# Optimization experiments

Measured on AMD Instinct MI355X. Metric: run time of the kernel, lower is better.

The kernel has to match this reference:

```python
import jax, jax.numpy as jnp
import numpy as np

N = 1_500_000
CB, CT, CO, B = 96, 128, 96, 8
BN_EPS = 1e-5


def setup_inputs() -> dict:
    key = jax.random.key(0)
    k1, k2, k3, k4 = jax.random.split(key, 4)
    return {
        "backbone_F": jax.random.normal(k1, (N, CB), dtype=jnp.float32),
        "batch_idx": jax.random.randint(k2, (N,), 0, B, dtype=jnp.int32),
        "text_feats": jax.random.normal(k3, (B, CT), dtype=jnp.float32),
        "W": jax.random.normal(k4, (CB + CT, CO), dtype=jnp.float32) * (1.0 / np.sqrt(CB + CT)),
        "gamma": jnp.ones((CO,), dtype=jnp.float32),
        "beta": jnp.zeros((CO,), dtype=jnp.float32),
    }


def reference(backbone_F, batch_idx, text_feats, W, gamma, beta):
    # gather text feats per point via batch index: [N, CT]
    rep_text = text_feats[batch_idx]
    # concat backbone + text feats: [N, CB+CT]
    combined = jnp.concatenate([backbone_F, rep_text], axis=1)
    # 1x1 sparse conv == pointwise GEMM (no bias): [N, CO]
    x = combined @ W
    # BatchNorm (training mode: batch stats over the N points)
    mean = jnp.mean(x, axis=0)
    var = jnp.var(x, axis=0)
    x = (x - mean) * jax.lax.rsqrt(var + BN_EPS) * gamma + beta
    # ReLU
    return jnp.maximum(x, 0.0)
```

## Files before the change

### kernel.cpp

```cpp
#include <hip/hip_runtime.h>
#include <hip/hip_bf16.h>

#define N_PTS 1500000
#define CBCH 96
#define CTCH 128
#define COCH 96
#define NB 8
#define BN_EPS 1e-5f

#define GSUM_OFF 0
#define GSQ_OFF 96
#define T_OFF 384

typedef __attribute__((ext_vector_type(8))) short bf16x8;
typedef __attribute__((ext_vector_type(4))) float f32x4;

__device__ __forceinline__ unsigned short f2bf_rne(float f) {
    union { float f; unsigned u; } v; v.f = f;
    unsigned u = v.u;
    return (unsigned short)((u + 0x7FFFu + ((u >> 16) & 1u)) >> 16);
}

__global__ void k0_init(const float* __restrict__ text, const float* __restrict__ W,
                        float* __restrict__ ws) {
    if (blockIdx.x == NB) {
        for (int i = threadIdx.x; i < 192; i += blockDim.x) ws[i] = 0.f;
        return;
    }
    int b = blockIdx.x;
    int c = threadIdx.x;
    if (c < COCH) {
        float acc = 0.f;
        #pragma unroll 8
        for (int k = 0; k < CTCH; ++k)
            acc += text[b * CTCH + k] * W[(CBCH + k) * COCH + c];
        ws[T_OFF + b * COCH + c] = acc;
    }
}


__device__ __forceinline__ void load_bfrag(const float* __restrict__ W, int grp, int lr,
                                           bf16x8 bf[6][3]) {
    #pragma unroll
    for (int ct = 0; ct < 6; ++ct)
        #pragma unroll
        for (int kt = 0; kt < 3; ++kt)
            #pragma unroll
            for (int j = 0; j < 8; ++j)
                bf[ct][kt][j] = (short)f2bf_rne(W[(kt * 32 + grp * 8 + j) * COCH + ct * 16 + lr]);
}

__global__ __launch_bounds__(256, 2) void k1_stats(const float* __restrict__ bb,
                                                   const int* __restrict__ bidx,
                                                   const float* __restrict__ W,
                                                   float* __restrict__ ws) {
    __shared__ float sT[NB * COCH];
    __shared__ float sred[2][4][COCH];
    for (int i = threadIdx.x; i < NB * COCH; i += blockDim.x) sT[i] = ws[T_OFF + i];
    __syncthreads();

    const int lane = threadIdx.x & 63;
    const int wv = threadIdx.x >> 6;
    const int grp = lane >> 4, lr = lane & 15;

    bf16x8 bf[6][3];
    load_bfrag(W, grp, lr, bf);

    float sum[6] = {0.f, 0.f, 0.f, 0.f, 0.f, 0.f};
    float sq[6] = {0.f, 0.f, 0.f, 0.f, 0.f, 0.f};

    const int gw = blockIdx.x * 4 + wv;
    const int nw = gridDim.x * 4;
    const int NT = N_PTS / 16;
    for (int t = gw; t < NT; t += nw) {
        int base = t * 16;
        f32x4 acc[6];
        #pragma unroll
        for (int r = 0; r < 4; ++r) {
            int b = bidx[base + grp * 4 + r];
            #pragma unroll
            for (int ct = 0; ct < 6; ++ct)
                acc[ct][r] = sT[b * COCH + ct * 16 + lr];
        }
        bf16x8 af[3];
        #pragma unroll
        for (int kt = 0; kt < 3; ++kt) {
            const f32x4* p = reinterpret_cast<const f32x4*>(bb + (size_t)(base + lr) * CBCH + kt * 32 + grp * 8);
            f32x4 x0 = p[0], x1 = p[1];
            #pragma unroll
            for (int j = 0; j < 4; ++j) {
                af[kt][j]     = (short)f2bf_rne(x0[j]);
                af[kt][4 + j] = (short)f2bf_rne(x1[j]);
            }
        }
        #pragma unroll
        for (int ct = 0; ct < 6; ++ct)
            #pragma unroll
            for (int kt = 0; kt < 3; ++kt)
                acc[ct] = __builtin_amdgcn_mfma_f32_16x16x32_bf16(af[kt], bf[ct][kt], acc[ct], 0, 0, 0);
        #pragma unroll
        for (int ct = 0; ct < 6; ++ct)
            #pragma unroll
            for (int r = 0; r < 4; ++r) {
                float x = acc[ct][r];
                sum[ct] += x;
                sq[ct] += x * x;
            }
    }

    #pragma unroll
    for (int ct = 0; ct < 6; ++ct) {
        float s = sum[ct], q = sq[ct];
        s += __shfl_xor(s, 16); q += __shfl_xor(q, 16);
        s += __shfl_xor(s, 32); q += __shfl_xor(q, 32);
        if (lane < 16) {
            sred[0][wv][ct * 16 + lane] = s;
            sred[1][wv][ct * 16 + lane] = q;
        }
    }
    __syncthreads();
    if (threadIdx.x < COCH) {
        int c = threadIdx.x;
        float s = sred[0][0][c] + sred[0][1][c] + sred[0][2][c] + sred[0][3][c];
        float q = sred[1][0][c] + sred[1][1][c] + sred[1][2][c] + sred[1][3][c];
        atomicAdd(&ws[GSUM_OFF + c], s);
        atomicAdd(&ws[GSQ_OFF + c], q);
    }
}

__global__ __launch_bounds__(256, 2) void k3_out(const float* __restrict__ bb,
                                                 const int* __restrict__ bidx,
                                                 const float* __restrict__ W,
                                                 const float* __restrict__ gamma,
                                                 const float* __restrict__ beta,
                                                 const float* __restrict__ ws,
                                                 float* __restrict__ out) {
    __shared__ float sT[NB * COCH];
    __shared__ float sScale[COCH];
    __shared__ float sBias[COCH];
    for (int i = threadIdx.x; i < NB * COCH; i += blockDim.x) sT[i] = ws[T_OFF + i];
    if (threadIdx.x < COCH) {
        int c = threadIdx.x;
        float mean = ws[GSUM_OFF + c] * (1.f / (float)N_PTS);
        float var  = ws[GSQ_OFF + c] * (1.f / (float)N_PTS) - mean * mean;
        float scl  = gamma[c] * rsqrtf(var + BN_EPS);
        sScale[c] = scl;
        sBias[c]  = beta[c] - mean * scl;
    }
    __syncthreads();

    const int lane = threadIdx.x & 63;
    const int wv = threadIdx.x >> 6;
    const int grp = lane >> 4, lr = lane & 15;

    bf16x8 bf[6][3];
    load_bfrag(W, grp, lr, bf);

    f32x4 sc[6], bs[6];
    #pragma unroll
    for (int ct = 0; ct < 6; ++ct) {
        sc[ct] = *reinterpret_cast<const f32x4*>(&sScale[ct * 16 + grp * 4]);
        bs[ct] = *reinterpret_cast<const f32x4*>(&sBias[ct * 16 + grp * 4]);
    }

    const int gw = blockIdx.x * 4 + wv;
    const int nw = gridDim.x * 4;
    const int NT = N_PTS / 16;
    for (int t = NT - 1 - gw; t >= 0; t -= nw) {
        int base = t * 16;
        int b = bidx[base + lr];
        f32x4 acc[6];
        #pragma unroll
        for (int ct = 0; ct < 6; ++ct)
            acc[ct] = *reinterpret_cast<const f32x4*>(&sT[b * COCH + ct * 16 + grp * 4]);

        bf16x8 pf[3];
        #pragma unroll
        for (int kt = 0; kt < 3; ++kt) {
            const f32x4* p = reinterpret_cast<const f32x4*>(bb + (size_t)(base + lr) * CBCH + kt * 32 + grp * 8);
            f32x4 x0 = __builtin_nontemporal_load(p);
            f32x4 x1 = __builtin_nontemporal_load(p + 1);
            #pragma unroll
            for (int j = 0; j < 4; ++j) {
                pf[kt][j]     = (short)f2bf_rne(x0[j]);
                pf[kt][4 + j] = (short)f2bf_rne(x1[j]);
            }
        }
        #pragma unroll
        for (int ct = 0; ct < 6; ++ct)
            #pragma unroll
            for (int kt = 0; kt < 3; ++kt)
                acc[ct] = __builtin_amdgcn_mfma_f32_16x16x32_bf16(bf[ct][kt], pf[kt], acc[ct], 0, 0, 0);

        #pragma unroll
        for (int ct = 0; ct < 6; ++ct) {
            f32x4 y;
            #pragma unroll
            for (int r = 0; r < 4; ++r)
                y[r] = fmaxf(acc[ct][r] * sc[ct][r] + bs[ct][r], 0.f);
            __builtin_nontemporal_store(y,
                reinterpret_cast<f32x4*>(out + (size_t)(base + lr) * COCH + ct * 16 + grp * 4));
        }
    }
}

extern "C" void kernel_launch(void* const* d_in, const int* in_sizes, int n_in,
                              void* d_out, int out_size, void* d_ws, size_t ws_size,
                              hipStream_t stream) {
    const float* bb    = (const float*)d_in[0];
    const int*   bidx  = (const int*)d_in[1];
    const float* text  = (const float*)d_in[2];
    const float* W     = (const float*)d_in[3];
    const float* gamma = (const float*)d_in[4];
    const float* beta  = (const float*)d_in[5];
    float* out = (float*)d_out;
    float* ws  = (float*)d_ws;

    hipLaunchKernelGGL(k0_init, dim3(NB + 1), dim3(128), 0, stream, text, W, ws);
    hipLaunchKernelGGL(k1_stats, dim3(2048), dim3(256), 0, stream, bb, bidx, W, ws);
    hipLaunchKernelGGL(k3_out, dim3(2048), dim3(256), 0, stream, bb, bidx, W, gamma, beta, ws, out);
}
```

Baseline: 376.4 us.

## Stage bf16 W fragments in LDS, share tile helper, shrink grid

W is converted to bf16 once per block into a fragment-ordered LDS array, and each lane then reads its B fragments with vector LDS loads instead of doing 144 strided global loads and conversions. The stats kernel now uses the same transposed MFMA orientation as the output kernel and accumulates f32x4 sums per row, followed by a different shuffle reduction. The text table in LDS is padded to reduce bank conflicts, the grid is cut from 2048 to 512 blocks, and the output kernel drops its nontemporal loads. The smaller grid lowers per-block setup cost and atomic traffic, but it may reduce latency hiding on the memory-bound streaming loop.

Measured after the change: 369.3 us. Within noise of the previous version (-1.9%).

```diff
diff --git a/kernel.cpp b/kernel.cpp
--- a/kernel.cpp
+++ b/kernel.cpp
@@ -2,11 +2,14 @@
 #include <hip/hip_bf16.h>
 
 #define N_PTS 1500000
+#define NT_TILES (N_PTS / 16)
 #define CBCH 96
 #define CTCH 128
 #define COCH 96
 #define NB 8
 #define BN_EPS 1e-5f
+#define GRID1 512
+#define STPAD 100
 
 #define GSUM_OFF 0
 #define GSQ_OFF 96
@@ -15,10 +18,11 @@
 typedef __attribute__((ext_vector_type(8))) short bf16x8;
 typedef __attribute__((ext_vector_type(4))) float f32x4;
 
-__device__ __forceinline__ unsigned short f2bf_rne(float f) {
-    union { float f; unsigned u; } v; v.f = f;
-    unsigned u = v.u;
-    return (unsigned short)((u + 0x7FFFu + ((u >> 16) & 1u)) >> 16);
+__device__ __forceinline__ short f2bf(float f) {
+    __hip_bfloat16 h = __float2bfloat16(f);
+    short s;
+    __builtin_memcpy(&s, &h, sizeof(s));
+    return s;
 }
 
 __global__ void k0_init(const float* __restrict__ text, const float* __restrict__ W,
@@ -39,24 +43,64 @@
 }
 
 
-__device__ __forceinline__ void load_bfrag(const float* __restrict__ W, int grp, int lr,
-                                           bf16x8 bf[6][3]) {
+__device__ __forceinline__ void stage_W(const float* __restrict__ W, short* sW) {
+    for (int i = threadIdx.x; i < CBCH * COCH; i += blockDim.x) {
+        int k = i / COCH, c = i % COCH;
+        int ct = c >> 4, lr = c & 15;
+        int kt = k >> 5, grp = (k >> 3) & 3, j = k & 7;
+        sW[(((ct * 3 + kt) * 64) + (grp * 16 + lr)) * 8 + j] = f2bf(W[i]);
+    }
+}
+
+__device__ __forceinline__ void load_bfrag_lds(const short* sW, int lane, bf16x8 bf[6][3]) {
     #pragma unroll
     for (int ct = 0; ct < 6; ++ct)
         #pragma unroll
         for (int kt = 0; kt < 3; ++kt)
-            #pragma unroll
-            for (int j = 0; j < 8; ++j)
-                bf[ct][kt][j] = (short)f2bf_rne(W[(kt * 32 + grp * 8 + j) * COCH + ct * 16 + lr]);
+            bf[ct][kt] = *reinterpret_cast<const bf16x8*>(sW + ((ct * 3 + kt) * 64 + lane) * 8);
+}
+
+__device__ __forceinline__ void tile_acc(const float* __restrict__ bb,
+                                         const int* __restrict__ bidx,
+                                         const float* __restrict__ sT,
+                                         const bf16x8 bf[6][3],
+                                         int base, int grp, int lr,
+                                         f32x4 acc[6]) {
+    int b = bidx[base + lr];
+    #pragma unroll
+    for (int ct = 0; ct < 6; ++ct)
+        acc[ct] = *reinterpret_cast<const f32x4*>(&sT[b * STPAD + ct * 16 + grp * 4]);
+
+    bf16x8 pf[3];
+    #pragma unroll
+    for (int kt = 0; kt < 3; ++kt) {
+        const f32x4* p = reinterpret_cast<const f32x4*>(bb + (size_t)(base + lr) * CBCH + kt * 32 + grp * 8);
+        f32x4 x0 = p[0], x1 = p[1];
+        #pragma unroll
+        for (int j = 0; j < 4; ++j) {
+            pf[kt][j]     = f2bf(x0[j]);
+            pf[kt][4 + j] = f2bf(x1[j]);
+        }
+    }
+    #pragma unroll
+    for (int ct = 0; ct < 6; ++ct)
+        #pragma unroll
+        for (int kt = 0; kt < 3; ++kt)
+            acc[ct] = __builtin_amdgcn_mfma_f32_16x16x32_bf16(bf[ct][kt], pf[kt], acc[ct], 0, 0, 0);
 }
 
 __global__ __launch_bounds__(256, 2) void k1_stats(const float* __restrict__ bb,
                                                    const int* __restrict__ bidx,
                                                    const float* __restrict__ W,
                                                    float* __restrict__ ws) {
-    __shared__ float sT[NB * COCH];
-    __shared__ float sred[2][4][COCH];
-    for (int i = threadIdx.x; i < NB * COCH; i += blockDim.x) sT[i] = ws[T_OFF + i];
+    __shared__ __align__(16) short sW[6 * 3 * 64 * 8];
+    __shared__ __align__(16) float sT[NB * STPAD];
+    __shared__ float sredS[4][COCH];
+    __shared__ float sredQ[4][COCH];
+
+    stage_W(W, sW);
+    for (int i = threadIdx.x; i < NB * COCH; i += blockDim.x)
+        sT[(i / COCH) * STPAD + (i % COCH)] = ws[T_OFF + i];
     __syncthreads();
 
     const int lane = threadIdx.x & 63;
@@ -64,67 +108,43 @@
     const int grp = lane >> 4, lr = lane & 15;
 
     bf16x8 bf[6][3];
-    load_bfrag(W, grp, lr, bf);
-
-    float sum[6] = {0.f, 0.f, 0.f, 0.f, 0.f, 0.f};
-    float sq[6] = {0.f, 0.f, 0.f, 0.f, 0.f, 0.f};
+    load_bfrag_lds(sW, lane, bf);
+
+    f32x4 sum[6], sq[6];
+    #pragma unroll
+    for (int ct = 0; ct < 6; ++ct) { sum[ct] = (f32x4)0.f; sq[ct] = (f32x4)0.f; }
 
     const int gw = blockIdx.x * 4 + wv;
-    const int nw = gridDim.x * 4;
-    const int NT = N_PTS / 16;
-    for (int t = gw; t < NT; t += nw) {
+    for (int t = gw; t < NT_TILES; t += GRID1 * 4) {
         int base = t * 16;
         f32x4 acc[6];
+        tile_acc(bb, bidx, sT, bf, base, grp, lr, acc);
+        #pragma unroll
+        for (int ct = 0; ct < 6; ++ct) {
+            sum[ct] += acc[ct];
+            sq[ct] += acc[ct] * acc[ct];
+        }
+    }
+
+    #pragma unroll
+    for (int ct = 0; ct < 6; ++ct)
         #pragma unroll
         for (int r = 0; r < 4; ++r) {
-            int b = bidx[base + grp * 4 + r];
-            #pragma unroll
-            for (int ct = 0; ct < 6; ++ct)
-                acc[ct][r] = sT[b * COCH + ct * 16 + lr];
-        }
-        bf16x8 af[3];
-        #pragma unroll
-        for (int kt = 0; kt < 3; ++kt) {
-            const f32x4* p = reinterpret_cast<const f32x4*>(bb + (size_t)(base + lr) * CBCH + kt * 32 + grp * 8);
-            f32x4 x0 = p[0], x1 = p[1];
-            #pragma unroll
-            for (int j = 0; j < 4; ++j) {
-                af[kt][j]     = (short)f2bf_rne(x0[j]);
-                af[kt][4 + j] = (short)f2bf_rne(x1[j]);
+            float s = sum[ct][r], q = sq[ct][r];
+            s += __shfl_xor(s, 1);  q += __shfl_xor(q, 1);
+            s += __shfl_xor(s, 2);  q += __shfl_xor(q, 2);
+            s += __shfl_xor(s, 4);  q += __shfl_xor(q, 4);
+            s += __shfl_xor(s, 8);  q += __shfl_xor(q, 8);
+            if (lr == 0) {
+                sredS[wv][ct * 16 + grp * 4 + r] = s;
+                sredQ[wv][ct * 16 + grp * 4 + r] = q;
             }
         }
-        #pragma unroll
-        for (int ct = 0; ct < 6; ++ct)
-            #pragma unroll
-            for (int kt = 0; kt < 3; ++kt)
-                acc[ct] = __builtin_amdgcn_mfma_f32_16x16x32_bf16(af[kt], bf[ct][kt], acc[ct], 0, 0, 0);
-        #pragma unroll
-        for (int ct = 0; ct < 6; ++ct)
-            #pragma unroll
-            for (int r = 0; r < 4; ++r) {
-                float x = acc[ct][r];
-                sum[ct] += x;
-                sq[ct] += x * x;
-            }
-    }
-
-    #pragma unroll
-    for (int ct = 0; ct < 6; ++ct) {
-        float s = sum[ct], q = sq[ct];
-        s += __shfl_xor(s, 16); q += __shfl_xor(q, 16);
-        s += __shfl_xor(s, 32); q += __shfl_xor(q, 32);
-        if (lane < 16) {
-            sred[0][wv][ct * 16 + lane] = s;
-            sred[1][wv][ct * 16 + lane] = q;
-        }
-    }
     __syncthreads();
     if (threadIdx.x < COCH) {
         int c = threadIdx.x;
-        float s = sred[0][0][c] + sred[0][1][c] + sred[0][2][c] + sred[0][3][c];
-        float q = sred[1][0][c] + sred[1][1][c] + sred[1][2][c] + sred[1][3][c];
-        atomicAdd(&ws[GSUM_OFF + c], s);
-        atomicAdd(&ws[GSQ_OFF + c], q);
+        atomicAdd(&ws[GSUM_OFF + c], sredS[0][c] + sredS[1][c] + sredS[2][c] + sredS[3][c]);
+        atomicAdd(&ws[GSQ_OFF + c],  sredQ[0][c] + sredQ[1][c] + sredQ[2][c] + sredQ[3][c]);
     }
 }
 
@@ -135,10 +155,14 @@
                                                  const float* __restrict__ beta,
                                                  const float* __restrict__ ws,
                                                  float* __restrict__ out) {
-    __shared__ float sT[NB * COCH];
-    __shared__ float sScale[COCH];
-    __shared__ float sBias[COCH];
-    for (int i = threadIdx.x; i < NB * COCH; i += blockDim.x) sT[i] = ws[T_OFF + i];
+    __shared__ __align__(16) short sW[6 * 3 * 64 * 8];
+    __shared__ __align__(16) float sT[NB * STPAD];
+    __shared__ __align__(16) float sScale[COCH];
+    __shared__ __align__(16) float sBias[COCH];
+
+    stage_W(W, sW);
+    for (int i = threadIdx.x; i < NB * COCH; i += blockDim.x)
+        sT[(i / COCH) * STPAD + (i % COCH)] = ws[T_OFF + i];
     if (threadIdx.x < COCH) {
         int c = threadIdx.x;
         float mean = ws[GSUM_OFF + c] * (1.f / (float)N_PTS);
@@ -154,7 +178,7 @@
     const int grp = lane >> 4, lr = lane & 15;
 
     bf16x8 bf[6][3];
-    load_bfrag(W, grp, lr, bf);
+    load_bfrag_lds(sW, lane, bf);
 
     f32x4 sc[6], bs[6];
     #pragma unroll
@@ -164,34 +188,10 @@
     }
 
     const int gw = blockIdx.x * 4 + wv;
-    const int nw = gridDim.x * 4;
-    const int NT = N_PTS / 16;
-    for (int t = NT - 1 - gw; t >= 0; t -= nw) {
+    for (int t = NT_TILES - 1 - gw; t >= 0; t -= GRID1 * 4) {
         int base = t * 16;
-        int b = bidx[base + lr];
         f32x4 acc[6];
-        #pragma unroll
-        for (int ct = 0; ct < 6; ++ct)
-            acc[ct] = *reinterpret_cast<const f32x4*>(&sT[b * COCH + ct * 16 + grp * 4]);
-
-        bf16x8 pf[3];
-        #pragma unroll
-        for (int kt = 0; kt < 3; ++kt) {
-            const f32x4* p = reinterpret_cast<const f32x4*>(bb + (size_t)(base + lr) * CBCH + kt * 32 + grp * 8);
-            f32x4 x0 = __builtin_nontemporal_load(p);
-            f32x4 x1 = __builtin_nontemporal_load(p + 1);
-            #pragma unroll
-            for (int j = 0; j < 4; ++j) {
-                pf[kt][j]     = (short)f2bf_rne(x0[j]);
-                pf[kt][4 + j] = (short)f2bf_rne(x1[j]);
-            }
-        }
-        #pragma unroll
-        for (int ct = 0; ct < 6; ++ct)
-            #pragma unroll
-            for (int kt = 0; kt < 3; ++kt)
-                acc[ct] = __builtin_amdgcn_mfma_f32_16x16x32_bf16(bf[ct][kt], pf[kt], acc[ct], 0, 0, 0);
-
+        tile_acc(bb, bidx, sT, bf, base, grp, lr, acc);
         #pragma unroll
         for (int ct = 0; ct < 6; ++ct) {
             f32x4 y;
@@ -217,6 +217,6 @@
     float* ws  = (float*)d_ws;
 
     hipLaunchKernelGGL(k0_init, dim3(NB + 1), dim3(128), 0, stream, text, W, ws);
-    hipLaunchKernelGGL(k1_stats, dim3(2048), dim3(256), 0, stream, bb, bidx, W, ws);
-    hipLaunchKernelGGL(k3_out, dim3(2048), dim3(256), 0, stream, bb, bidx, W, gamma, beta, ws, out);
-}
+    hipLaunchKernelGGL(k1_stats, dim3(GRID1), dim3(256), 0, stream, bb, bidx, W, ws);
+    hipLaunchKernelGGL(k3_out, dim3(GRID1), dim3(256), 0, stream, bb, bidx, W, gamma, beta, ws, out);
+}
```
